# Kernel optimization log

Measured on AMD Instinct MI355X. Metric: run time of the kernel, lower is better.

The kernel has to match this reference:

```python
import jax, jax.numpy as jnp
import numpy as np

B, S, D = 2, 512, 256      # batch, seq_len, d_model
N = 16                     # d_state
DC = 4                     # d_conv
DI = 2 * D                 # d_inner
CHUNK = 32                 # scan remat chunk size (S % CHUNK == 0)


def setup_inputs() -> dict:
    key = jax.random.key(0)
    ks = jax.random.split(key, 10)
    sc = 0.02
    return {
        "x": jax.random.normal(ks[0], (B, S, D), jnp.float32),
        "adjacency_matrix": jax.random.uniform(ks[1], (B, S, S), dtype=jnp.float32),
        "ln_w": jnp.ones((D,), jnp.float32),
        "ln_b": jnp.zeros((D,), jnp.float32),
        "W_in": jax.random.normal(ks[2], (2 * DI, D), jnp.float32) * sc,
        "conv_w": jax.random.normal(ks[3], (DI, DI, DC), jnp.float32) * sc,
        "conv_b": jnp.zeros((DI,), jnp.float32),
        "W_xp": jax.random.normal(ks[4], (2 * N + 1, DI), jnp.float32) * sc,
        "W_dt": jax.random.normal(ks[5], (DI, 1), jnp.float32) * sc,
        "b_dt": jnp.zeros((DI,), jnp.float32),
        "Wr": jax.random.normal(ks[6], (N, N), jnp.float32) * sc,
        "br": jnp.zeros((N,), jnp.float32),
        "W_out": jax.random.normal(ks[7], (D, DI), jnp.float32) * sc,
    }


def _forward(x, adj, ln_w, ln_b, W_in, conv_w, conv_b, W_xp, W_dt, b_dt, Wr, br, W_out):
    residual = x
    # LayerNorm (biased variance, eps=1e-5, matching nn.LayerNorm)
    mu = x.mean(-1, keepdims=True)
    var = ((x - mu) ** 2).mean(-1, keepdims=True)
    xn = (x - mu) * jax.lax.rsqrt(var + 1e-5) * ln_w + ln_b
    # in_proj (no bias), chunk into x branch and gate z
    xz = xn @ W_in.T                                  # [B,S,2*DI]
    xp, z = xz[..., :DI], xz[..., DI:]
    # causal-ish conv1d with padding d_conv-1, then slice to seq_len
    xc = jax.lax.conv_general_dilated(
        xp.transpose(0, 2, 1), conv_w, (1,), [(DC - 1, DC - 1)],
        dimension_numbers=("NCH", "OIH", "NCH"))
    xc = (xc + conv_b[None, :, None])[..., :S].transpose(0, 2, 1)  # [B,S,DI]
    x_act = jax.nn.silu(xc)
    # x_proj (no bias) -> delta(1), B(N), C(N)
    ssm = x_act @ W_xp.T                              # [B,S,2N+1]
    delta = jax.nn.softplus(ssm[..., :1] @ W_dt.T + b_dt)  # [B,S,DI]
    Bm, Cm = ssm[..., 1:1 + N], ssm[..., 1 + N:]      # [B,S,N]
    pos = jnp.arange(S)

    def step(carry, xs):
        h, hist = xs_carry = carry
        t, d_t, B_t, C_t, x_t, a_t = xs
        # exponential-decay state update: h [B,DI,N]
        h = h * jnp.exp(-d_t)[..., None] + x_t[..., None] * B_t[:, None, :]
        # adjacency-gated, degree-normalized aggregation over prior states
        w = a_t * (pos < t)                           # [B,S], zeros for s>=t
        deg = jnp.maximum(w.sum(-1), 1.0)             # clamp(min=1.0)
        g = jnp.einsum('bs,sbdn->bdn', w, hist) / deg[:, None, None]
        boost = 0.1 * jax.nn.silu(g @ Wr.T + br)
        # torch skips the boost when t==0 or all causal weights are zero
        h = h + jnp.where((t > 0) & jnp.any(w > 0), boost, jnp.zeros_like(boost))
        hist = hist.at[t].set(h)
        y = jnp.einsum('bdn,bn->bd', h, C_t)
        return (h, hist), y

    xs = (pos,
          delta.transpose(1, 0, 2), Bm.transpose(1, 0, 2), Cm.transpose(1, 0, 2),
          x_act.transpose(1, 0, 2), adj.transpose(1, 0, 2))
    nchunks = S // CHUNK
    xs = jax.tree_util.tree_map(lambda a: a.reshape(nchunks, CHUNK, *a.shape[1:]), xs)
    carry0 = (jnp.zeros((B, DI, N), jnp.float32),
              jnp.zeros((S, B, DI, N), jnp.float32))

    @jax.checkpoint
    def chunk_body(carry, xs_c):
        return jax.lax.scan(step, carry, xs_c)

    _, ys = jax.lax.scan(chunk_body, carry0, xs)
    y = ys.reshape(S, B, DI).transpose(1, 0, 2)       # [B,S,DI]
    return (y * jax.nn.silu(z)) @ W_out.T + residual


def reference(x, adjacency_matrix, ln_w, ln_b, W_in, conv_w, conv_b, W_xp, W_dt, b_dt, Wr, br, W_out):
    return _forward(x, adjacency_matrix, ln_w, ln_b, W_in, conv_w, conv_b,
                    W_xp, W_dt, b_dt, Wr, br, W_out)
```

## Files before the change

kernel.cpp:

```cpp
#include <hip/hip_runtime.h>
#include <math.h>

static constexpr int B  = 2;
static constexpr int S  = 512;
static constexpr int D  = 256;
static constexpr int N  = 16;
static constexpr int DI = 512;
static constexpr int CHUNK = 32;
static constexpr int NCHUNK = S / CHUNK;
static constexpr int NL2 = 4;
static constexpr int DN = DI * N;
static constexpr int NSLOT = 8;

typedef unsigned int uint32;
typedef unsigned short ushort16;
using bf16x8 = __attribute__((ext_vector_type(8))) short;
using f32x4  = __attribute__((ext_vector_type(4))) float;

__device__ __forceinline__ ushort16 f2bf(float f) {
    uint32 u = __float_as_uint(f);
    u = (u + 0x7fffu + ((u >> 16) & 1u)) >> 16;
    return (ushort16)u;
}
__device__ __forceinline__ float bflo(uint32 u) { return __uint_as_float(u << 16); }
__device__ __forceinline__ float bfhi(uint32 u) { return __uint_as_float(u & 0xffff0000u); }
__device__ __forceinline__ float bf2f(ushort16 u) { return __uint_as_float(((uint32)u) << 16); }
__device__ __forceinline__ uint32 pk2(float a, float b) {
    return (uint32)(ushort16)f2bf(a) | ((uint32)(ushort16)f2bf(b) << 16);
}
template<int K>
__device__ __forceinline__ float rork(float x) {
    return __uint_as_float((uint32)__builtin_amdgcn_mov_dpp(
        (int)__float_as_uint(x), 0x120 + K, 0xf, 0xf, false));
}
__device__ __forceinline__ size_t htIdx(int b, int dn, int sb) {
    return ((size_t)(b * (S / 32) + sb) * DN + dn) * 32;
}

__global__ void ln_k(const float* __restrict__ x, const float* __restrict__ w,
                     const float* __restrict__ bias, ushort16* __restrict__ xnb) {
    int row = blockIdx.x;
    int lane = threadIdx.x;
    float4 v = *(const float4*)(x + row * D + lane * 4);
    float s = v.x + v.y + v.z + v.w;
    float q = v.x * v.x + v.y * v.y + v.z * v.z + v.w * v.w;
    for (int m = 1; m < 64; m <<= 1) { s += __shfl_xor(s, m); q += __shfl_xor(q, m); }
    float mu  = s * (1.0f / D);
    float var = q * (1.0f / D) - mu * mu;
    float rs  = rsqrtf(var + 1e-5f);
    float4 wv = *(const float4*)(w + lane * 4);
    float4 bv = *(const float4*)(bias + lane * 4);
    float4 o;
    o.x = (v.x - mu) * rs * wv.x + bv.x;
    o.y = (v.y - mu) * rs * wv.y + bv.y;
    o.z = (v.z - mu) * rs * wv.z + bv.z;
    o.w = (v.w - mu) * rs * wv.w + bv.w;
    uint2 pk;
    pk.x = pk2(o.x, o.y);
    pk.y = pk2(o.z, o.w);
    *(uint2*)(xnb + row * D + lane * 4) = pk;
}

template<int MODE>
__global__ __launch_bounds__(256) void gemmb_k(const ushort16* __restrict__ A,
                                               const float* __restrict__ W,
                                               const float* __restrict__ res,
                                               float* __restrict__ C,
                                               ushort16* __restrict__ xpb,
                                               float* __restrict__ zs,
                                               int M, int Nc, int K) {
    __shared__ __align__(16) short As[64 * 40];
    __shared__ __align__(16) short Ws[64 * 40];
    int tid = threadIdx.x;
    int l = tid & 63, wid = tid >> 6;
    int wm = wid & 1, wn = wid >> 1;
    int row0 = blockIdx.y * 64, col0 = blockIdx.x * 64;
    int r = tid >> 2, kseg = (tid & 3) * 8;
    f32x4 acc[2][2] = {};
    for (int k0 = 0; k0 < K; k0 += 32) {
        *(uint4*)&As[r * 40 + kseg] = *(const uint4*)(A + (size_t)(row0 + r) * K + k0 + kseg);
        {
            const float* wrow = W + (size_t)(col0 + r) * K + k0 + kseg;
            float4 w0 = *(const float4*)wrow;
            float4 w1 = *(const float4*)(wrow + 4);
            uint4 q;
            q.x = pk2(w0.x, w0.y); q.y = pk2(w0.z, w0.w);
            q.z = pk2(w1.x, w1.y); q.w = pk2(w1.z, w1.w);
            *(uint4*)&Ws[r * 40 + kseg] = q;
        }
        __syncthreads();
        bf16x8 aF[2], bF[2];
        #pragma unroll
        for (int am = 0; am < 2; ++am)
            aF[am] = *(const bf16x8*)&As[(wm * 32 + am * 16 + (l & 15)) * 40 + (l >> 4) * 8];
        #pragma unroll
        for (int bn = 0; bn < 2; ++bn)
            bF[bn] = *(const bf16x8*)&Ws[(wn * 32 + bn * 16 + (l & 15)) * 40 + (l >> 4) * 8];
        #pragma unroll
        for (int am = 0; am < 2; ++am)
            #pragma unroll
            for (int bn = 0; bn < 2; ++bn)
                acc[am][bn] = __builtin_amdgcn_mfma_f32_16x16x32_bf16(aF[am], bF[bn], acc[am][bn], 0, 0, 0);
        __syncthreads();
    }
    #pragma unroll
    for (int am = 0; am < 2; ++am)
        #pragma unroll
        for (int bn = 0; bn < 2; ++bn) {
            int cc = col0 + wn * 32 + bn * 16 + (l & 15);
            #pragma unroll
            for (int reg = 0; reg < 4; ++reg) {
                int rr = row0 + wm * 32 + am * 16 + (l >> 4) * 4 + reg;
                float v = acc[am][bn][reg];
                if (MODE == 0) {
                    if (res) v += res[(size_t)rr * Nc + cc];
                    C[(size_t)rr * Nc + cc] = v;
                } else {
                    int b = rr >> 9, t = rr & (S - 1);
                    if (cc < DI)
                        xpb[((size_t)(b * (S + 3) + 3 + t)) * DI + cc] = f2bf(v);
                    else
                        zs[((size_t)(b * S + t)) * DI + (cc - DI)] = v / (1.0f + __expf(-v));
                }
            }
        }
}

__global__ __launch_bounds__(256) void convm_k(const ushort16* __restrict__ xpb,
                                               const float* __restrict__ conv_w,
                                               const float* __restrict__ conv_b,
                                               float* __restrict__ x_act) {
    __shared__ __align__(16) short AxS[35 * 40];
    __shared__ __align__(16) short WbS[4 * 32 * 40];
    int tid = threadIdx.x;
    int l = tid & 63, wid = tid >> 6;
    int wm = wid & 1, wn = wid >> 1;
    int o0 = blockIdx.x * 32;
    int mt = blockIdx.y;
    int b = mt >> 4, tl0 = (mt & 15) * 32;
    f32x4 acc = {0.f, 0.f, 0.f, 0.f};

    for (int k0 = 0; k0 < DI; k0 += 32) {
        if (tid < 140) {
            int rr = tid >> 2, seg = tid & 3;
            uint4 v = *(const uint4*)(xpb + ((size_t)(b * (S + 3) + tl0 + rr)) * DI + k0 + seg * 8);
            *(uint4*)&AxS[rr * 40 + seg * 8] = v;
        }
        #pragma unroll
        for (int it = 0; it < 4; ++it) {
            int p = it * 256 + tid;
            int o = p >> 5, i = p & 31;
            float4 w4 = *(const float4*)(conv_w + ((size_t)(o0 + o) * DI + (k0 + i)) * 4);
            WbS[(0 * 32 + o) * 40 + i] = (short)f2bf(w4.x);
            WbS[(1 * 32 + o) * 40 + i] = (short)f2bf(w4.y);
            WbS[(2 * 32 + o) * 40 + i] = (short)f2bf(w4.z);
            WbS[(3 * 32 + o) * 40 + i] = (short)f2bf(w4.w);
        }
        __syncthreads();
        #pragma unroll
        for (int k = 0; k < 4; ++k) {
            bf16x8 aF = *(const bf16x8*)&AxS[(wm * 16 + (l & 15) + k) * 40 + (l >> 4) * 8];
            bf16x8 bF = *(const bf16x8*)&WbS[(k * 32 + wn * 16 + (l & 15)) * 40 + (l >> 4) * 8];
            acc = __builtin_amdgcn_mfma_f32_16x16x32_bf16(aF, bF, acc, 0, 0, 0);
        }
        __syncthreads();
    }
    int oc = o0 + wn * 16 + (l & 15);
    float bia = conv_b[oc];
    #pragma unroll
    for (int reg = 0; reg < 4; ++reg) {
        int m = wm * 16 + (l >> 4) * 4 + reg;
        float v = acc[reg] + bia;
        x_act[((size_t)(b * S + tl0 + m)) * DI + oc] = v / (1.0f + __expf(-v));
    }
}

__global__ void ssmE_k(const float* __restrict__ x_act, const float* __restrict__ W_xp,
                       const float* __restrict__ W_dt, const float* __restrict__ b_dt,
                       float* __restrict__ Bm, float* __restrict__ Cm,
                       float* __restrict__ E) {
    int row = blockIdx.x * 4 + (threadIdx.x >> 6);
    int lane = threadIdx.x & 63;
    const float* xr = x_act + (size_t)row * DI + lane * 8;
    float4 v0 = *(const float4*)xr;
    float4 v1 = *(const float4*)(xr + 4);
    float dtr = 0.0f;
    for (int j = 0; j < 2 * N + 1; ++j) {
        const float* wr = W_xp + (size_t)j * DI + lane * 8;
        float4 w0 = *(const float4*)wr;
        float4 w1 = *(const float4*)(wr + 4);
        float acc = v0.x * w0.x + v0.y * w0.y + v0.z * w0.z + v0.w * w0.w
                  + v1.x * w1.x + v1.y * w1.y + v1.z * w1.z + v1.w * w1.w;
        for (int m = 1; m < 64; m <<= 1) acc += __shfl_xor(acc, m);
        if (j == 0) dtr = acc;
        if (lane == 0) {
            if (j >= 1 && j < 1 + N) Bm[(size_t)row * N + (j - 1)] = acc;
            else if (j >= 1 + N)     Cm[(size_t)row * N + (j - 1 - N)] = acc;
        }
    }
    int d0 = lane * 8;
    float4 w0 = *(const float4*)(W_dt + d0);
    float4 w1 = *(const float4*)(W_dt + d0 + 4);
    float4 q0 = *(const float4*)(b_dt + d0);
    float4 q1 = *(const float4*)(b_dt + d0 + 4);
    float4 e0, e1;
    e0.x = 1.0f / (1.0f + __expf(dtr * w0.x + q0.x));
    e0.y = 1.0f / (1.0f + __expf(dtr * w0.y + q0.y));
    e0.z = 1.0f / (1.0f + __expf(dtr * w0.z + q0.z));
    e0.w = 1.0f / (1.0f + __expf(dtr * w0.w + q0.w));
    e1.x = 1.0f / (1.0f + __expf(dtr * w1.x + q1.x));
    e1.y = 1.0f / (1.0f + __expf(dtr * w1.y + q1.y));
    e1.z = 1.0f / (1.0f + __expf(dtr * w1.z + q1.z));
    e1.w = 1.0f / (1.0f + __expf(dtr * w1.w + q1.w));
    *(float4*)(E + (size_t)row * DI + d0) = e0;
    *(float4*)(E + (size_t)row * DI + d0 + 4) = e1;
}

__global__ void deg_k(const float* __restrict__ adj, float* __restrict__ rdeg, int* __restrict__ flagI) {
    int t = blockIdx.x & (S - 1), b = blockIdx.x >> 9;
    int lane = threadIdx.x;
    const float* row = adj + ((size_t)(b * S + t)) * S;
    float s = 0.0f; bool anyp = false;
    for (int i = lane; i < t; i += 64) { float v = row[i]; s += v; anyp |= (v > 0.0f); }
    for (int m = 1; m < 64; m <<= 1) s += __shfl_xor(s, m);
    bool any = __any(anyp);
    if (lane == 0) {
        rdeg[b * S + t] = 1.0f / fmaxf(s, 1.0f);
        if (t > 0 && any) atomicOr(flagI + t, 1);
    }
}

#define SCAN32(RO, ADJT, GSUM)                                              \
    _Pragma("unroll")                                                       \
    for (int j = 0; j < CHUNK; ++j) {                                       \
        float e  = eL [((RO) + j) * 8 + grp];                               \
        float xa = xaL[((RO) + j) * 8 + grp];                               \
        float Bn = BnL[((RO) + j) * 16 + n];                                \
        h = h * e + xa * Bn;                                                \
        float g0 = GSUM[j], g1 = 0.f, g2 = 0.f, g3 = 0.f;                   \
        const float* ar = (ADJT) + j * 36;                                  \
        int sp = 0;                                                         \
        _Pragma("unroll")                                                   \
        for (; sp + 4 <= j; sp += 4) {                                      \
            float4 av = *(const float4*)(ar + sp);                          \
            g0 += av.x * hreg[sp];     g1 += av.y * hreg[sp + 1];           \
            g2 += av.z * hreg[sp + 2]; g3 += av.w * hreg[sp + 3];           \
        }                                                                   \
        _Pragma("unroll")                                                   \
        for (; sp < j; ++sp) g0 += ar[sp] * hreg[sp];                       \
        float gr = (g0 + g1) + (g2 + g3);                                   \
        float m0 = gr * wrr[0] + rork<4>(gr) * wrr[4]                       \
                 + rork<8>(gr) * wrr[8] + rork<12>(gr) * wrr[12];           \
        float m1 = rork<1>(gr) * wrr[1] + rork<5>(gr) * wrr[5]              \
                 + rork<9>(gr) * wrr[9] + rork<13>(gr) * wrr[13];           \
        float m2 = rork<2>(gr) * wrr[2] + rork<6>(gr) * wrr[6]              \
                 + rork<10>(gr) * wrr[10] + rork<14>(gr) * wrr[14];         \
        float m3 = rork<3>(gr) * wrr[3] + rork<7>(gr) * wrr[7]              \
                 + rork<11>(gr) * wrr[11] + rork<15>(gr) * wrr[15];         \
        float acc = fmaf(rdegL[(RO) + j], (m0 + m1) + (m2 + m3), brn);      \
        if (flL[(RO) + j])                                                  \
            h = fmaf(0.1f * acc,                                            \
                     __builtin_amdgcn_rcpf(1.0f + __expf(-acc)), h);        \
        hreg[j] = h;                                                        \
    }

#define PRESUM(GSUM, PTR) {                                                 \
    const ushort16* _p = (PTR);                                             \
    _Pragma("unroll")                                                       \
    for (int qi = 0; qi < 4; ++qi) {                                        \
        uint4 q = *(const uint4*)(_p + qi * 8);                             \
        GSUM[qi*8+0] += bflo(q.x); GSUM[qi*8+1] += bfhi(q.x);               \
        GSUM[qi*8+2] += bflo(q.y); GSUM[qi*8+3] += bfhi(q.y);               \
        GSUM[qi*8+4] += bflo(q.z); GSUM[qi*8+5] += bfhi(q.z);               \
        GSUM[qi*8+6] += bflo(q.w); GSUM[qi*8+7] += bfhi(q.w);               \
    } }

#define HWRITE(CIDX, HTBUF) {                                               \
    ushort16* ht = histT + htIdx(b, dn, (CIDX));                            \
    _Pragma("unroll")                                                       \
    for (int qi = 0; qi < 4; ++qi) {                                        \
        uint4 q;                                                            \
        q.x = pk2(hreg[qi*8+0], hreg[qi*8+1]);                              \
        q.y = pk2(hreg[qi*8+2], hreg[qi*8+3]);                              \
        q.z = pk2(hreg[qi*8+4], hreg[qi*8+5]);                              \
        q.w = pk2(hreg[qi*8+6], hreg[qi*8+7]);                              \
        *(uint4*)(ht + qi * 8) = q;                                         \
        *(uint4*)&(HTBUF)[qi * 1024 + tid * 8] = q;                         \
    } }

#define MIDPHASE(TCL) {                                                     \
    int w = tid >> 6, l = tid & 63;                                         \
    int ksg = (l >> 4) * 8;                                                 \
    f32x4 ac0[4] = {}, ac1[4] = {};                                         \
    _Pragma("unroll")                                                       \
    for (int sidx = 0; sidx < (TCL); ++sidx) {                              \
        const float* p0 = adj + ((size_t)(b * S + c0s + (TCL) * 32 + (l & 15))) * S \
                        + c0s + sidx * 32 + ksg;                            \
        const float* p1 = p0 + 16 * S;                                      \
        float4 a00 = *(const float4*)p0, a01 = *(const float4*)(p0 + 4);    \
        float4 a10 = *(const float4*)p1, a11 = *(const float4*)(p1 + 4);    \
        uint4 qa, qb;                                                       \
        qa.x = pk2(a00.x, a00.y); qa.y = pk2(a00.z, a00.w);                 \
        qa.z = pk2(a01.x, a01.y); qa.w = pk2(a01.z, a01.w);                 \
        qb.x = pk2(a10.x, a10.y); qb.y = pk2(a10.z, a10.w);                 \
        qb.z = pk2(a11.x, a11.y); qb.w = pk2(a11.z, a11.w);                 \
        bf16x8 aF0, aF1;                                                    \
        *(uint4*)&aF0 = qa; *(uint4*)&aF1 = qb;                             \
        const short* hTs = hTarr[sidx];                                     \
        _Pragma("unroll")                                                   \
        for (int dblk = 0; dblk < 4; ++dblk) {                              \
            int col = w * 64 + dblk * 16 + (l & 15);                        \
            bf16x8 bF = *(const bf16x8*)&hTs[(l >> 4) * 1024 + col * 8];    \
            ac0[dblk] = __builtin_amdgcn_mfma_f32_16x16x32_bf16(aF0, bF, ac0[dblk], 0, 0, 0); \
            ac1[dblk] = __builtin_amdgcn_mfma_f32_16x16x32_bf16(aF1, bF, ac1[dblk], 0, 0, 0); \
        }                                                                   \
    }                                                                       \
    int jb0 = (l >> 4) * 4;                                                 \
    _Pragma("unroll")                                                       \
    for (int dblk = 0; dblk < 4; ++dblk) {                                  \
        int col = w * 64 + dblk * 16 + (l & 15);                            \
        _Pragma("unroll")                                                   \
        for (int reg = 0; reg < 4; ++reg) {                                 \
            Gmid[(jb0 + reg) * 136 + col]      = (short)f2bf(ac0[dblk][reg]); \
            Gmid[(16 + jb0 + reg) * 136 + col] = (short)f2bf(ac1[dblk][reg]); \
        }                                                                   \
    } }

#define GSADD(GSUM)                                                         \
    _Pragma("unroll")                                                       \
    for (int j = 0; j < CHUNK; ++j)                                         \
        GSUM[j] += bf2f((ushort16)Gmid[j * 136 + tid]);

__global__ __launch_bounds__(256) void chunk4_k(const float* __restrict__ adj,
                                                const float* __restrict__ x_act,
                                                const float* __restrict__ E,
                                                const float* __restrict__ Bm,
                                                const float* __restrict__ rdeg,
                                                const int* __restrict__ flagI,
                                                const float* __restrict__ Wr,
                                                const float* __restrict__ br,
                                                ushort16* __restrict__ Gall,
                                                ushort16* __restrict__ histT,
                                                float* __restrict__ hlast, int lc) {
    __shared__ __align__(16) char smem[51200];
    int tid = threadIdx.x;
    int c0 = 4 * lc;
    int c0s = c0 * CHUNK;
    const size_t SLOT = (size_t)B * DN * 32;
    int rp = lc & 1, wp = (lc + 1) & 1;

    if (blockIdx.x < 128) {
        float* triA  = (float*)smem;
        float* triB  = (float*)(smem + 4608);
        float* eL    = (float*)(smem + 9216);
        float* xaL   = (float*)(smem + 11264);
        float* BnL   = (float*)(smem + 13312);
        float* rdegL = (float*)(smem + 17408);
        int*   flL   = (int*)  (smem + 17664);
        short* hTA   = (short*)(smem + 17920);
        short* hTB   = (short*)(smem + 26112);
        short* hTC   = (short*)(smem + 34304);
        short* Gmid  = (short*)(smem + 42496);
        short* hTD   = (short*)(smem + 42496);

        int b = blockIdx.x >> 6;
        int d0 = (blockIdx.x & 63) << 3;
        int n = tid & 15, grp = (tid >> 4) & 7;
        int d = d0 + grp;
        int dn = d * N + n;
        int dnbase = (blockIdx.x & 63) << 7;
        const short* hTarr[4] = {hTA, hTB, hTC, hTD};

        {
            int j = tid >> 3, s4 = (tid & 7) * 4;
            {
                float4 a0 = *(const float4*)(adj + ((size_t)(b * S + c0s + j)) * S + c0s + s4);
                float* dp = triA + j * 36 + s4;
                dp[0] = a0.x; dp[1] = a0.y; dp[2] = a0.z; dp[3] = a0.w;
            }
            {
                float4 a0 = *(const float4*)(adj + ((size_t)(b * S + c0s + 32 + j)) * S + c0s + 32 + s4);
                float* dp = triB + j * 36 + s4;
                dp[0] = a0.x; dp[1] = a0.y; dp[2] = a0.z; dp[3] = a0.w;
            }
            int jr = tid >> 2, dd = (tid & 3) * 2;
            float2 ev = *(const float2*)(E     + ((size_t)(b * S + c0s + jr)) * DI + d0 + dd);
            float2 xv = *(const float2*)(x_act + ((size_t)(b * S + c0s + jr)) * DI + d0 + dd);
            eL [jr * 8 + dd] = ev.x; eL [jr * 8 + dd + 1] = ev.y;
            xaL[jr * 8 + dd] = xv.x; xaL[jr * 8 + dd + 1] = xv.y;
            int nn = (tid & 3) * 4;
            float4 bv = *(const float4*)(Bm + ((size_t)(b * S + c0s + jr)) * N + nn);
            BnL[jr * 16 + nn] = bv.x; BnL[jr * 16 + nn + 1] = bv.y;
            BnL[jr * 16 + nn + 2] = bv.z; BnL[jr * 16 + nn + 3] = bv.w;
            if (tid < 64) {
                rdegL[tid] = rdeg[b * S + c0s + tid];
                flL[tid]   = flagI[c0s + tid];
            }
        }
        __syncthreads();

        float gs0[CHUNK], gs1[CHUNK];
        float wrr[16];
        float brn = 0.f, h = 0.f;
        float hreg[CHUNK];

        if (tid < 128) {
            #pragma unroll
            for (int j = 0; j < CHUNK; ++j) { gs0[j] = 0.f; gs1[j] = 0.f; }
            size_t tb = ((size_t)b * DN + dn) * 32;
            if (lc >= 2) {
                PRESUM(gs0, Gall + ((size_t)rp * NSLOT + 0) * SLOT + tb);
                PRESUM(gs1, Gall + ((size_t)rp * NSLOT + 1) * SLOT + tb);
            }
            if (lc >= 1) {
                PRESUM(gs0, Gall + ((size_t)rp * NSLOT + 4) * SLOT + tb);
                PRESUM(gs1, Gall + ((size_t)rp * NSLOT + 5) * SLOT + tb);
            }
            int probe = __builtin_amdgcn_mov_dpp((int)n, 0x121, 0xf, 0xf, false);
            bool plusdir = (probe == ((n + 1) & 15));
            #pragma unroll
            for (int k = 0; k < 16; ++k) {
                int ip = (n + k) & 15, im = (n - k + 16) & 15;
                wrr[k] = Wr[n * 16 + (plusdir ? ip : im)];
            }
            brn = br[n];
            h = (lc == 0) ? 0.0f : hlast[b * DN + dn];

            SCAN32(0, triA, gs0)
            HWRITE(c0 + 0, hTA)
        }
        __syncthreads();
        if (tid < 128) MIDPHASE(1)
        __syncthreads();
        if (tid < 128) {
            GSADD(gs1)
            SCAN32(32, triB, gs1)
            HWRITE(c0 + 1, hTB)
        }
        __syncthreads();

        {
            int j = tid >> 3, s4 = (tid & 7) * 4;
            {
                float4 a0 = *(const float4*)(adj + ((size_t)(b * S + c0s + 64 + j)) * S + c0s + 64 + s4);
                float* dp = triA + j * 36 + s4;
                dp[0] = a0.x; dp[1] = a0.y; dp[2] = a0.z; dp[3] = a0.w;
            }
            {
                float4 a0 = *(const float4*)(adj + ((size_t)(b * S + c0s + 96 + j)) * S + c0s + 96 + s4);
                float* dp = triB + j * 36 + s4;
                dp[0] = a0.x; dp[1] = a0.y; dp[2] = a0.z; dp[3] = a0.w;
            }
            int jr = tid >> 2, dd = (tid & 3) * 2;
            float2 ev = *(const float2*)(E     + ((size_t)(b * S + c0s + 64 + jr)) * DI + d0 + dd);
            float2 xv = *(const float2*)(x_act + ((size_t)(b * S + c0s + 64 + jr)) * DI + d0 + dd);
            eL [jr * 8 + dd] = ev.x; eL [jr * 8 + dd + 1] = ev.y;
            xaL[jr * 8 + dd] = xv.x; xaL[jr * 8 + dd + 1] = xv.y;
            int nn = (tid & 3) * 4;
            float4 bv = *(const float4*)(Bm + ((size_t)(b * S + c0s + 64 + jr)) * N + nn);
            BnL[jr * 16 + nn] = bv.x; BnL[jr * 16 + nn + 1] = bv.y;
            BnL[jr * 16 + nn + 2] = bv.z; BnL[jr * 16 + nn + 3] = bv.w;
            if (tid < 64) {
                rdegL[tid] = rdeg[b * S + c0s + 64 + tid];
                flL[tid]   = flagI[c0s + 64 + tid];
            }
        }
        if (tid < 128) {
            #pragma unroll
            for (int j = 0; j < CHUNK; ++j) { gs0[j] = 0.f; gs1[j] = 0.f; }
            size_t tb = ((size_t)b * DN + dn) * 32;
            if (lc >= 2) {
                PRESUM(gs0, Gall + ((size_t)rp * NSLOT + 2) * SLOT + tb);
                PRESUM(gs1, Gall + ((size_t)rp * NSLOT + 3) * SLOT + tb);
            }
            if (lc >= 1) {
                PRESUM(gs0, Gall + ((size_t)rp * NSLOT + 6) * SLOT + tb);
                PRESUM(gs1, Gall + ((size_t)rp * NSLOT + 7) * SLOT + tb);
            }
        }
        __syncthreads();
        if (tid < 128) MIDPHASE(2)
        __syncthreads();
        if (tid < 128) {
            GSADD(gs0)
            SCAN32(0, triA, gs0)
            HWRITE(c0 + 2, hTC)
        }
        __syncthreads();
        if (tid < 128) MIDPHASE(3)
        __syncthreads();
        if (tid < 128) GSADD(gs1)
        __syncthreads();
        if (tid < 128) {
            SCAN32(32, triB, gs1)
            HWRITE(c0 + 3, hTD)
            hlast[b * DN + dn] = h;
        }
        __syncthreads();

        if (lc < NL2 - 1) {
            int half = tid >> 7;
            int lt = tid & 127;
            int w = lt >> 6, l = lt & 63;
            int ksg = (l >> 4) * 8;
            int jb0 = (l >> 4) * 4;
            #pragma unroll
            for (int tp = 0; tp < 2; ++tp) {
                int tgt = half * 2 + tp;
                f32x4 ac0[4] = {}, ac1[4] = {};
                #pragma unroll
                for (int src = 0; src < 4; ++src) {
                    const short* hTs = hTarr[src];
                    const float* p0 = adj + ((size_t)(b * S + (4 * (lc + 1) + tgt) * 32 + (l & 15))) * S
                                    + (4 * lc + src) * 32 + ksg;
                    const float* p1 = p0 + 16 * S;
                    float4 a00 = *(const float4*)p0, a01 = *(const float4*)(p0 + 4);
                    float4 a10 = *(const float4*)p1, a11 = *(const float4*)(p1 + 4);
                    uint4 qa, qb;
                    qa.x = pk2(a00.x, a00.y); qa.y = pk2(a00.z, a00.w);
                    qa.z = pk2(a01.x, a01.y); qa.w = pk2(a01.z, a01.w);
                    qb.x = pk2(a10.x, a10.y); qb.y = pk2(a10.z, a10.w);
                    qb.z = pk2(a11.x, a11.y); qb.w = pk2(a11.z, a11.w);
                    bf16x8 aF0, aF1;
                    *(uint4*)&aF0 = qa; *(uint4*)&aF1 = qb;
                    #pragma unroll
                    for (int dblk = 0; dblk < 4; ++dblk) {
                        int col = w * 64 + dblk * 16 + (l & 15);
                        bf16x8 bF = *(const bf16x8*)&hTs[(l >> 4) * 1024 + col * 8];
                        ac0[dblk] = __builtin_amdgcn_mfma_f32_16x16x32_bf16(aF0, bF, ac0[dblk], 0, 0, 0);
                        ac1[dblk] = __builtin_amdgcn_mfma_f32_16x16x32_bf16(aF1, bF, ac1[dblk], 0, 0, 0);
                    }
                }
                ushort16* gw = Gall + ((size_t)wp * NSLOT + (4 + tgt)) * SLOT;
                #pragma unroll
                for (int dblk = 0; dblk < 4; ++dblk) {
                    int col = w * 64 + dblk * 16 + (l & 15);
                    int dng = dnbase + col;
                    uint2 o0, o1;
                    o0.x = pk2(ac0[dblk][0], ac0[dblk][1]); o0.y = pk2(ac0[dblk][2], ac0[dblk][3]);
                    o1.x = pk2(ac1[dblk][0], ac1[dblk][1]); o1.y = pk2(ac1[dblk][2], ac1[dblk][3]);
                    *(uint2*)(gw + ((size_t)b * DN + dng) * 32 + jb0) = o0;
                    *(uint2*)(gw + ((size_t)b * DN + dng) * 32 + 16 + jb0) = o1;
                }
            }
        }
    } else {
        if (lc == 0 || lc >= NL2 - 1) return;
        int idx = blockIdx.x - 128;
        int tile = idx & 63;
        int b = idx >> 6;
        int dn0 = tile * 128;
        int w = tid >> 6, l = tid & 63;
        int jh = w & 1, dh = w >> 1;
        int ksg = (l >> 4) * 8;
        int dnrow = dn0 + dh * 64 + (l & 15);
        int K = 4 * lc;
        const float* abase0 = adj + ((size_t)(b * S + (4 * (lc + 1) + 0) * CHUNK + jh * 16 + (l & 15))) * S + ksg;
        const float* abase1 = abase0 + (size_t)CHUNK * S;
        const float* abase2 = abase1 + (size_t)CHUNK * S;
        const float* abase3 = abase2 + (size_t)CHUNK * S;
        f32x4 acc[4][4] = {};
        #pragma unroll 1
        for (int ks = 0; ks < K; ++ks) {
            bf16x8 bF[4];
            #pragma unroll
            for (int dblk = 0; dblk < 4; ++dblk) {
                uint4 bP = *(const uint4*)(histT + htIdx(b, dnrow + dblk * 16, ks) + ksg);
                *(uint4*)&bF[dblk] = bP;
            }
            #pragma unroll
            for (int tgt = 0; tgt < 4; ++tgt) {
                const float* ab = (tgt == 0) ? abase0 : (tgt == 1) ? abase1
                                : (tgt == 2) ? abase2 : abase3;
                float4 af0 = *(const float4*)(ab + ks * 32);
                float4 af1 = *(const float4*)(ab + ks * 32 + 4);
                uint4 aP;
                aP.x = pk2(af0.x, af0.y); aP.y = pk2(af0.z, af0.w);
                aP.z = pk2(af1.x, af1.y); aP.w = pk2(af1.z, af1.w);
                bf16x8 aF;
                *(uint4*)&aF = aP;
                #pragma unroll
                for (int dblk = 0; dblk < 4; ++dblk)
                    acc[tgt][dblk] = __builtin_amdgcn_mfma_f32_16x16x32_bf16(aF, bF[dblk], acc[tgt][dblk], 0, 0, 0);
            }
        }
        int jb = jh * 16 + (l >> 4) * 4;
        #pragma unroll
        for (int tgt = 0; tgt < 4; ++tgt) {
            ushort16* gbase = Gall + ((size_t)wp * NSLOT + tgt) * SLOT;
            #pragma unroll
            for (int dblk = 0; dblk < 4; ++dblk) {
                int dnc = dn0 + dh * 64 + dblk * 16 + (l & 15);
                uint2 o;
                o.x = pk2(acc[tgt][dblk][0], acc[tgt][dblk][1]);
                o.y = pk2(acc[tgt][dblk][2], acc[tgt][dblk][3]);
                *(uint2*)(gbase + ((size_t)b * DN + dnc) * 32 + jb) = o;
            }
        }
    }
}

__global__ __launch_bounds__(256) void y_k(const ushort16* __restrict__ histT,
                                           const float* __restrict__ Cm,
                                           const float* __restrict__ zs,
                                           ushort16* __restrict__ yzb) {
    __shared__ float CmL[S * 17];
    int b = blockIdx.x >> 9;
    int d = blockIdx.x & (DI - 1);
    int tid = threadIdx.x;
    #pragma unroll
    for (int q = 0; q < 8; ++q) {
        int l0 = q * 1024 + tid * 4;
        int t = l0 >> 4, n0 = l0 & 15;
        float4 v = *(const float4*)(Cm + (size_t)b * S * N + l0);
        CmL[t * 17 + n0]     = v.x;
        CmL[t * 17 + n0 + 1] = v.y;
        CmL[t * 17 + n0 + 2] = v.z;
        CmL[t * 17 + n0 + 3] = v.w;
    }
    __syncthreads();
    #pragma unroll
    for (int pass = 0; pass < 2; ++pass) {
        int t = pass * 256 + tid;
        int sb = t >> 5, si = t & 31;
        const ushort16* hb = histT + htIdx(b, d * N, sb) + si;
        float a0 = 0.f, a1 = 0.f, a2 = 0.f, a3 = 0.f;
        #pragma unroll
        for (int n = 0; n < 16; n += 4) {
            a0 += bf2f(hb[(size_t)n * 32])       * CmL[t * 17 + n];
            a1 += bf2f(hb[(size_t)(n + 1) * 32]) * CmL[t * 17 + n + 1];
            a2 += bf2f(hb[(size_t)(n + 2) * 32]) * CmL[t * 17 + n + 2];
            a3 += bf2f(hb[(size_t)(n + 3) * 32]) * CmL[t * 17 + n + 3];
        }
        float acc = (a0 + a1) + (a2 + a3);
        float zv = zs[((size_t)(b * S + t)) * DI + d];
        yzb[((size_t)(b * S + t)) * DI + d] = f2bf(acc * zv);
    }
}

extern "C" void kernel_launch(void* const* d_in, const int* in_sizes, int n_in,
                              void* d_out, int out_size, void* d_ws, size_t ws_size,
                              hipStream_t stream) {
    const float* x      = (const float*)d_in[0];
    const float* adj    = (const float*)d_in[1];
    const float* ln_w   = (const float*)d_in[2];
    const float* ln_b   = (const float*)d_in[3];
    const float* W_in   = (const float*)d_in[4];
    const float* conv_w = (const float*)d_in[5];
    const float* conv_b = (const float*)d_in[6];
    const float* W_xp   = (const float*)d_in[7];
    const float* W_dt   = (const float*)d_in[8];
    const float* b_dt   = (const float*)d_in[9];
    const float* Wr     = (const float*)d_in[10];
    const float* br     = (const float*)d_in[11];
    const float* W_out  = (const float*)d_in[12];
    float* out = (float*)d_out;

    float* ws = (float*)d_ws;
    size_t off = 0;
    float* x_act  = ws + off; off += (size_t)B * S * DI;
    float* Bmb    = ws + off; off += (size_t)B * S * N;
    float* Cmb    = ws + off; off += (size_t)B * S * N;
    float* rdegp  = ws + off; off += (size_t)B * S;
    int*   flagI  = (int*)(ws + off); off += S;
    float* Ebuf   = ws + off; off += (size_t)B * S * DI;
    float* zsbuf  = ws + off; off += (size_t)B * S * DI;
    float* hlast  = ws + off; off += (size_t)B * DN;
    ushort16* xnb    = (ushort16*)(ws + off); off += (size_t)B * S * D / 2;
    ushort16* yzb    = (ushort16*)(ws + off); off += (size_t)B * S * DI / 2;
    ushort16* histT  = (ushort16*)(ws + off); off += (size_t)B * DN * S / 2;
    ushort16* Gall   = (ushort16*)(ws + off); off += (size_t)2 * NSLOT * B * DN * 32 / 2;
    ushort16* xpb    = (ushort16*)(ws + off); off += (size_t)B * (S + 3) * DI / 2;

    hipMemsetAsync(flagI, 0, S * sizeof(int), stream);
    hipMemsetAsync(xpb, 0, (size_t)B * (S + 3) * DI * 2, stream);

    ln_k<<<B * S, 64, 0, stream>>>(x, ln_w, ln_b, xnb);
    gemmb_k<1><<<dim3(2 * DI / 64, B * S / 64), 256, 0, stream>>>(
        xnb, W_in, nullptr, nullptr, xpb, zsbuf, B * S, 2 * DI, D);
    convm_k<<<dim3(DI / 32, B * S / 32), 256, 0, stream>>>(xpb, conv_w, conv_b, x_act);
    ssmE_k<<<B * S / 4, 256, 0, stream>>>(x_act, W_xp, W_dt, b_dt, Bmb, Cmb, Ebuf);
    deg_k<<<B * S, 64, 0, stream>>>(adj, rdegp, flagI);

    for (int lc = 0; lc < NL2; ++lc)
        chunk4_k<<<256, 256, 0, stream>>>(adj, x_act, Ebuf, Bmb, rdegp, flagI,
                                          Wr, br, Gall, histT, hlast, lc);

    y_k<<<B * DI, 256, 0, stream>>>(histT, Cmb, zsbuf, yzb);

    gemmb_k<0><<<dim3(D / 64, B * S / 64), 256, 0, stream>>>(
        yzb, W_out, x, out, nullptr, nullptr, B * S, D, DI);
}
```

Baseline: 259.2 us.

## Double-buffer chunk staging so idle threads prefetch the second half during scan

Result: no change. 256.9 us (-0.9%).

```diff
diff --git a/kernel.cpp b/kernel.cpp
--- a/kernel.cpp
+++ b/kernel.cpp
@@ -230,12 +230,12 @@
     }
 }
 
-#define SCAN32(RO, ADJT, GSUM)                                              \
+#define SCAN32(RO, ADJT, GSUM, EL, XAL, BNL, RDEGL, FLL)                    \
     _Pragma("unroll")                                                       \
     for (int j = 0; j < CHUNK; ++j) {                                       \
-        float e  = eL [((RO) + j) * 8 + grp];                               \
-        float xa = xaL[((RO) + j) * 8 + grp];                               \
-        float Bn = BnL[((RO) + j) * 16 + n];                                \
+        float e  = (EL) [((RO) + j) * 8 + grp];                             \
+        float xa = (XAL)[((RO) + j) * 8 + grp];                             \
+        float Bn = (BNL)[((RO) + j) * 16 + n];                              \
         h = h * e + xa * Bn;                                                \
         float g0 = GSUM[j], g1 = 0.f, g2 = 0.f, g3 = 0.f;                   \
         const float* ar = (ADJT) + j * 36;                                  \
@@ -257,8 +257,8 @@
                  + rork<10>(gr) * wrr[10] + rork<14>(gr) * wrr[14];         \
         float m3 = rork<3>(gr) * wrr[3] + rork<7>(gr) * wrr[7]              \
                  + rork<11>(gr) * wrr[11] + rork<15>(gr) * wrr[15];         \
-        float acc = fmaf(rdegL[(RO) + j], (m0 + m1) + (m2 + m3), brn);      \
-        if (flL[(RO) + j])                                                  \
+        float acc = fmaf((RDEGL)[(RO) + j], (m0 + m1) + (m2 + m3), brn);    \
+        if ((FLL)[(RO) + j])                                                \
             h = fmaf(0.1f * acc,                                            \
                      __builtin_amdgcn_rcpf(1.0f + __expf(-acc)), h);        \
         hreg[j] = h;                                                        \
@@ -331,6 +331,32 @@
     for (int j = 0; j < CHUNK; ++j)                                         \
         GSUM[j] += bf2f((ushort16)Gmid[j * 136 + tid]);
 
+#define STAGEOPS(T, OFS, TRI0, TRI1, EL, XAL, BNL, RDEGL, FLL) {            \
+    int j = (T) >> 3, s4 = ((T) & 7) * 4;                                   \
+    {                                                                       \
+        float4 a0 = *(const float4*)(adj + ((size_t)(b * S + c0s + (OFS) + j)) * S + c0s + (OFS) + s4); \
+        float* dp = (TRI0) + j * 36 + s4;                                   \
+        dp[0] = a0.x; dp[1] = a0.y; dp[2] = a0.z; dp[3] = a0.w;             \
+    }                                                                       \
+    {                                                                       \
+        float4 a0 = *(const float4*)(adj + ((size_t)(b * S + c0s + (OFS) + 32 + j)) * S + c0s + (OFS) + 32 + s4); \
+        float* dp = (TRI1) + j * 36 + s4;                                   \
+        dp[0] = a0.x; dp[1] = a0.y; dp[2] = a0.z; dp[3] = a0.w;             \
+    }                                                                       \
+    int jr = (T) >> 2, dd = ((T) & 3) * 2;                                  \
+    float2 ev = *(const float2*)(E     + ((size_t)(b * S + c0s + (OFS) + jr)) * DI + d0 + dd); \
+    float2 xv = *(const float2*)(x_act + ((size_t)(b * S + c0s + (OFS) + jr)) * DI + d0 + dd); \
+    (EL) [jr * 8 + dd] = ev.x; (EL) [jr * 8 + dd + 1] = ev.y;               \
+    (XAL)[jr * 8 + dd] = xv.x; (XAL)[jr * 8 + dd + 1] = xv.y;               \
+    int nn = ((T) & 3) * 4;                                                 \
+    float4 bv = *(const float4*)(Bm + ((size_t)(b * S + c0s + (OFS) + jr)) * N + nn); \
+    (BNL)[jr * 16 + nn] = bv.x; (BNL)[jr * 16 + nn + 1] = bv.y;             \
+    (BNL)[jr * 16 + nn + 2] = bv.z; (BNL)[jr * 16 + nn + 3] = bv.w;         \
+    if ((T) < 64) {                                                         \
+        (RDEGL)[(T)] = rdeg[b * S + c0s + (OFS) + (T)];                     \
+        (FLL)[(T)]   = flagI[c0s + (OFS) + (T)];                            \
+    } }
+
 __global__ __launch_bounds__(256) void chunk4_k(const float* __restrict__ adj,
                                                 const float* __restrict__ x_act,
                                                 const float* __restrict__ E,
@@ -342,7 +368,7 @@
                                                 ushort16* __restrict__ Gall,
                                                 ushort16* __restrict__ histT,
                                                 float* __restrict__ hlast, int lc) {
-    __shared__ __align__(16) char smem[51200];
+    __shared__ __align__(16) char smem[69120];
     int tid = threadIdx.x;
     int c0 = 4 * lc;
     int c0s = c0 * CHUNK;
@@ -350,18 +376,25 @@
     int rp = lc & 1, wp = (lc + 1) & 1;
 
     if (blockIdx.x < 128) {
-        float* triA  = (float*)smem;
-        float* triB  = (float*)(smem + 4608);
-        float* eL    = (float*)(smem + 9216);
-        float* xaL   = (float*)(smem + 11264);
-        float* BnL   = (float*)(smem + 13312);
-        float* rdegL = (float*)(smem + 17408);
-        int*   flL   = (int*)  (smem + 17664);
-        short* hTA   = (short*)(smem + 17920);
-        short* hTB   = (short*)(smem + 26112);
-        short* hTC   = (short*)(smem + 34304);
-        short* Gmid  = (short*)(smem + 42496);
-        short* hTD   = (short*)(smem + 42496);
+        float* triA   = (float*)smem;
+        float* triB   = (float*)(smem + 4608);
+        float* eLa    = (float*)(smem + 9216);
+        float* xaLa   = (float*)(smem + 11264);
+        float* BnLa   = (float*)(smem + 13312);
+        float* rdegLa = (float*)(smem + 17408);
+        int*   flLa   = (int*)  (smem + 17664);
+        float* triC   = (float*)(smem + 17920);
+        float* triD   = (float*)(smem + 22528);
+        float* eLb    = (float*)(smem + 27136);
+        float* xaLb   = (float*)(smem + 29184);
+        float* BnLb   = (float*)(smem + 31232);
+        float* rdegLb = (float*)(smem + 35328);
+        int*   flLb   = (int*)  (smem + 35584);
+        short* hTA    = (short*)(smem + 35840);
+        short* hTB    = (short*)(smem + 44032);
+        short* hTC    = (short*)(smem + 52224);
+        short* Gmid   = (short*)(smem + 60416);
+        short* hTD    = (short*)(smem + 60416);
 
         int b = blockIdx.x >> 6;
         int d0 = (blockIdx.x & 63) << 3;
@@ -371,32 +404,7 @@
         int dnbase = (blockIdx.x & 63) << 7;
         const short* hTarr[4] = {hTA, hTB, hTC, hTD};
 
-        {
-            int j = tid >> 3, s4 = (tid & 7) * 4;
-            {
-                float4 a0 = *(const float4*)(adj + ((size_t)(b * S + c0s + j)) * S + c0s + s4);
-                float* dp = triA + j * 36 + s4;
-                dp[0] = a0.x; dp[1] = a0.y; dp[2] = a0.z; dp[3] = a0.w;
-            }
-            {
-                float4 a0 = *(const float4*)(adj + ((size_t)(b * S + c0s + 32 + j)) * S + c0s + 32 + s4);
-                float* dp = triB + j * 36 + s4;
-                dp[0] = a0.x; dp[1] = a0.y; dp[2] = a0.z; dp[3] = a0.w;
-            }
-            int jr = tid >> 2, dd = (tid & 3) * 2;
-            float2 ev = *(const float2*)(E     + ((size_t)(b * S + c0s + jr)) * DI + d0 + dd);
-            float2 xv = *(const float2*)(x_act + ((size_t)(b * S + c0s + jr)) * DI + d0 + dd);
-            eL [jr * 8 + dd] = ev.x; eL [jr * 8 + dd + 1] = ev.y;
-            xaL[jr * 8 + dd] = xv.x; xaL[jr * 8 + dd + 1] = xv.y;
-            int nn = (tid & 3) * 4;
-            float4 bv = *(const float4*)(Bm + ((size_t)(b * S + c0s + jr)) * N + nn);
-            BnL[jr * 16 + nn] = bv.x; BnL[jr * 16 + nn + 1] = bv.y;
-            BnL[jr * 16 + nn + 2] = bv.z; BnL[jr * 16 + nn + 3] = bv.w;
-            if (tid < 64) {
-                rdegL[tid] = rdeg[b * S + c0s + tid];
-                flL[tid]   = flagI[c0s + tid];
-            }
-        }
+        STAGEOPS(tid, 0, triA, triB, eLa, xaLa, BnLa, rdegLa, flLa)
         __syncthreads();
 
         float gs0[CHUNK], gs1[CHUNK];
@@ -426,45 +434,25 @@
             brn = br[n];
             h = (lc == 0) ? 0.0f : hlast[b * DN + dn];
 
-            SCAN32(0, triA, gs0)
+            SCAN32(0, triA, gs0, eLa, xaLa, BnLa, rdegLa, flLa)
             HWRITE(c0 + 0, hTA)
+        } else {
+            #pragma unroll
+            for (int rep = 0; rep < 2; ++rep) {
+                int t2 = ((tid - 128) << 1) | rep;
+                STAGEOPS(t2, 64, triC, triD, eLb, xaLb, BnLb, rdegLb, flLb)
+            }
         }
         __syncthreads();
         if (tid < 128) MIDPHASE(1)
         __syncthreads();
         if (tid < 128) {
             GSADD(gs1)
-            SCAN32(32, triB, gs1)
+            SCAN32(32, triB, gs1, eLa, xaLa, BnLa, rdegLa, flLa)
             HWRITE(c0 + 1, hTB)
         }
         __syncthreads();
 
-        {
-            int j = tid >> 3, s4 = (tid & 7) * 4;
-            {
-                float4 a0 = *(const float4*)(adj + ((size_t)(b * S + c0s + 64 + j)) * S + c0s + 64 + s4);
-                float* dp = triA + j * 36 + s4;
-                dp[0] = a0.x; dp[1] = a0.y; dp[2] = a0.z; dp[3] = a0.w;
-            }
-            {
-                float4 a0 = *(const float4*)(adj + ((size_t)(b * S + c0s + 96 + j)) * S + c0s + 96 + s4);
-                float* dp = triB + j * 36 + s4;
-                dp[0] = a0.x; dp[1] = a0.y; dp[2] = a0.z; dp[3] = a0.w;
-            }
-            int jr = tid >> 2, dd = (tid & 3) * 2;
-            float2 ev = *(const float2*)(E     + ((size_t)(b * S + c0s + 64 + jr)) * DI + d0 + dd);
-            float2 xv = *(const float2*)(x_act + ((size_t)(b * S + c0s + 64 + jr)) * DI + d0 + dd);
-            eL [jr * 8 + dd] = ev.x; eL [jr * 8 + dd + 1] = ev.y;
-            xaL[jr * 8 + dd] = xv.x; xaL[jr * 8 + dd + 1] = xv.y;
-            int nn = (tid & 3) * 4;
-            float4 bv = *(const float4*)(Bm + ((size_t)(b * S + c0s + 64 + jr)) * N + nn);
-            BnL[jr * 16 + nn] = bv.x; BnL[jr * 16 + nn + 1] = bv.y;
-            BnL[jr * 16 + nn + 2] = bv.z; BnL[jr * 16 + nn + 3] = bv.w;
-            if (tid < 64) {
-                rdegL[tid] = rdeg[b * S + c0s + 64 + tid];
-                flL[tid]   = flagI[c0s + 64 + tid];
-            }
-        }
         if (tid < 128) {
             #pragma unroll
             for (int j = 0; j < CHUNK; ++j) { gs0[j] = 0.f; gs1[j] = 0.f; }
@@ -477,13 +465,12 @@
                 PRESUM(gs0, Gall + ((size_t)rp * NSLOT + 6) * SLOT + tb);
                 PRESUM(gs1, Gall + ((size_t)rp * NSLOT + 7) * SLOT + tb);
             }
-        }
-        __syncthreads();
-        if (tid < 128) MIDPHASE(2)
+            MIDPHASE(2)
+        }
         __syncthreads();
         if (tid < 128) {
             GSADD(gs0)
-            SCAN32(0, triA, gs0)
+            SCAN32(0, triC, gs0, eLb, xaLb, BnLb, rdegLb, flLb)
             HWRITE(c0 + 2, hTC)
         }
         __syncthreads();
@@ -492,7 +479,7 @@
         if (tid < 128) GSADD(gs1)
         __syncthreads();
         if (tid < 128) {
-            SCAN32(32, triB, gs1)
+            SCAN32(32, triD, gs1, eLb, xaLb, BnLb, rdegLb, flLb)
             HWRITE(c0 + 3, hTD)
             hlast[b * DN + dn] = h;
         }
```
